# Kernel optimization log

Measured on AMD Instinct MI355X. Metric: run time of the kernel, lower is better.

## Reference

```python
import jax, jax.numpy as jnp
import numpy as np

B, N, HID = 2, 2048, 768
H, D, W = 12, 64, 128  # heads, head_dim, attention_half_width
P = 2 * W + 1          # number of relative-position buckets


def setup_inputs() -> dict:
    key = jax.random.key(0)
    ks = jax.random.split(key, 8)
    s = 0.02
    return {
        "hidden_states": jax.random.normal(ks[0], (B, N, HID), jnp.float32),
        "attention_mask": jnp.ones((B, N), jnp.bool_),
        "Wq": jax.random.normal(ks[1], (HID, HID), jnp.float32) * s,
        "Wk": jax.random.normal(ks[2], (HID, HID), jnp.float32) * s,
        "Wv": jax.random.normal(ks[3], (HID, HID), jnp.float32) * s,
        "position_query": jax.random.normal(ks[4], (1, H, D, P), jnp.float32),
        "position_key": jax.random.normal(ks[5], (1, H, D, P), jnp.float32),
        "Wo": jax.random.normal(ks[6], (HID, HID), jnp.float32) * s,
        "bo": jnp.zeros((HID,), jnp.float32),
    }


def reference(hidden_states, attention_mask, Wq, Wk, Wv, position_query, position_key, Wo, bo):
    b, n, hid = hidden_states.shape
    h, d, p = position_query.shape[1], position_query.shape[2], position_query.shape[3]
    w = (p - 1) // 2

    def split_heads(x):
        return x.reshape(b, n, h, d).transpose(0, 2, 1, 3)  # [B,H,N,D]

    q = split_heads(hidden_states @ Wq.T)
    k = split_heads(hidden_states @ Wk.T)
    v = split_heads(hidden_states @ Wv.T)

    # content-content scores (no sqrt(d) scaling in the original)
    score = jnp.einsum("bhid,bhjd->bhij", q, k)

    # relative position index: idx[i,j] = clip(j - i + w, 0, 2w)
    ids = jnp.arange(n)
    idx = jnp.clip(ids[None, :] - ids[:, None] + w, 0, 2 * w)  # [N,N] int32
    idx4 = idx[None, None]  # broadcast over B,H

    # content-to-position: gather over relative buckets
    c2p = jnp.einsum("bhid,hdp->bhip", q, position_key[0])  # [B,H,N,P]
    score = score + jnp.take_along_axis(c2p, idx4, axis=-1)

    # position-to-content: gather then transpose last two dims
    p2c = jnp.einsum("bhjd,hdp->bhjp", k, position_query[0])  # [B,H,N,P]
    score = score + jnp.swapaxes(jnp.take_along_axis(p2c, idx4, axis=-1), -1, -2)

    # band mask (|i-j| <= w) AND key/query validity masks
    band = jnp.abs(ids[:, None] - ids[None, :]) <= w  # [N,N]
    am = attention_mask.astype(jnp.bool_)
    mask = band[None, None] & am[:, None, None, :] & am[:, None, :, None]

    lv = jnp.finfo(score.dtype).min
    score = score + lv * (~mask).astype(score.dtype)  # additive masking, as in torch

    proba = jax.nn.softmax(score, axis=-1)
    context = jnp.einsum("bhij,bhjd->bhid", proba, v)
    context = context.transpose(0, 2, 1, 3).reshape(b, n, h * d)

    # VariationalNormalEpanechnikovDropout is identity in eval mode
    output = context @ Wo.T + bo
    return output, proba
```

## Files before the change

kernel.cpp:

```cpp
#include <hip/hip_runtime.h>
#include <math.h>

constexpr int kB   = 2;
constexpr int kN   = 2048;
constexpr int kHid = 768;
constexpr int kH   = 12;
constexpr int kD   = 64;
constexpr int kW   = 128;
constexpr int kP   = 2 * kW + 1;
constexpr int kPp  = 320;
constexpr int kM   = kB * kN;
constexpr int BHND = kB * kH * kN * kD;
constexpr int BHNP = kB * kH * kN * kP;

using f16 = _Float16;
typedef _Float16 f16x8 __attribute__((ext_vector_type(8)));
typedef _Float16 f16x4 __attribute__((ext_vector_type(4)));
typedef float    f32x4 __attribute__((ext_vector_type(4)));

__device__ __forceinline__ f16 f2h(float f) { return (f16)f; }
__device__ __forceinline__ float h2f(f16 h) { return (float)h; }
__device__ __forceinline__ void gload_lds16(const void* g, void* lds) {
  __builtin_amdgcn_global_load_lds((const __attribute__((address_space(1))) unsigned int*)g,
                                   (__attribute__((address_space(3))) unsigned int*)lds, 16, 0, 0);
}

__global__ __launch_bounds__(256) void castf2h(const float4* __restrict__ in,
                                               f16x4* __restrict__ out, int n4) {
  for (int i = blockIdx.x * 256 + threadIdx.x; i < n4; i += gridDim.x * 256) {
    const float4 f = in[i];
    f16x4 u;
    u[0] = f2h(f.x); u[1] = f2h(f.y); u[2] = f2h(f.z); u[3] = f2h(f.w);
    out[i] = u;
  }
}

__global__ __launch_bounds__(256) void cast4(const float* __restrict__ a, const float* __restrict__ b,
                                             const float* __restrict__ c, const float* __restrict__ d,
                                             f16* __restrict__ oa, f16* __restrict__ ob,
                                             f16* __restrict__ oc, f16* __restrict__ od) {
  const float* src[4] = {a, b, c, d};
  f16*         dst[4] = {oa, ob, oc, od};
  const int y = blockIdx.y;
  const int i = blockIdx.x * 256 + threadIdx.x;
  const float4 f = ((const float4*)src[y])[i];
  f16x4 u;
  u[0] = f2h(f.x); u[1] = f2h(f.y); u[2] = f2h(f.z); u[3] = f2h(f.w);
  ((f16x4*)dst[y])[i] = u;
}

__global__ __launch_bounds__(256) void postrans(const float* __restrict__ pq, const float* __restrict__ pk,
                                                f16* __restrict__ pqt, f16* __restrict__ pkt) {
  const float* s = blockIdx.y ? pk : pq;
  f16*         o = blockIdx.y ? pkt : pqt;
  const int idx = blockIdx.x * 256 + threadIdx.x;
  const int h = idx / (kPp * kD);
  const int rem = idx % (kPp * kD);
  const int p = rem >> 6, d = rem & 63;
  const float v = (p < kP) ? s[((size_t)h * kD + d) * kP + p] : 0.f;
  o[idx] = f2h(v);
}

template <int MODE>
__global__ __launch_bounds__(256) void gemm_mfma(const f16* __restrict__ A,
                                                 const f16* __restrict__ Bt,
                                                 const float* __restrict__ bias,
                                                 float* __restrict__ outF,
                                                 f16* __restrict__ outB) {
  __shared__ f16 Ab[2][64 * 32];
  __shared__ f16 Bb[2][64 * 32];
  const int tid = threadIdx.x;
  const int lane = tid & 63, wave = tid >> 6;
  const int wm = wave >> 1, wn = wave & 1;
  const int m0 = blockIdx.y * 64, c0 = blockIdx.x * 64;

  const int srow = tid >> 2, sseg = (tid & 3) * 8;
  const f16* gA = A + (size_t)(m0 + srow) * kHid + sseg;
  const f16* gB = Bt + (size_t)(c0 + srow) * kHid + sseg;

  f32x4 acc[2][2] = {};
  const int fr = lane & 15, fk = (lane >> 4) * 8;

  gload_lds16(gA, &Ab[0][wave * 512]);
  gload_lds16(gB, &Bb[0][wave * 512]);
  __syncthreads();

  int cur = 0;
  for (int t = 0; t < 24; ++t) {
    if (t < 23) {
      gload_lds16(gA + (t + 1) * 32, &Ab[cur ^ 1][wave * 512]);
      gload_lds16(gB + (t + 1) * 32, &Bb[cur ^ 1][wave * 512]);
    }
    const f16x8 a0 = *(const f16x8*)&Ab[cur][(wm * 32 + fr) * 32 + fk];
    const f16x8 a1 = *(const f16x8*)&Ab[cur][(wm * 32 + 16 + fr) * 32 + fk];
    const f16x8 b0 = *(const f16x8*)&Bb[cur][(wn * 32 + fr) * 32 + fk];
    const f16x8 b1 = *(const f16x8*)&Bb[cur][(wn * 32 + 16 + fr) * 32 + fk];
    acc[0][0] = __builtin_amdgcn_mfma_f32_16x16x32_f16(a0, b0, acc[0][0], 0, 0, 0);
    acc[0][1] = __builtin_amdgcn_mfma_f32_16x16x32_f16(a0, b1, acc[0][1], 0, 0, 0);
    acc[1][0] = __builtin_amdgcn_mfma_f32_16x16x32_f16(a1, b0, acc[1][0], 0, 0, 0);
    acc[1][1] = __builtin_amdgcn_mfma_f32_16x16x32_f16(a1, b1, acc[1][1], 0, 0, 0);
    __syncthreads();
    cur ^= 1;
  }

  const int orow0 = m0 + wm * 32 + (lane >> 4) * 4;
  const int ocol0 = c0 + wn * 32 + (lane & 15);
#pragma unroll
  for (int m16 = 0; m16 < 2; ++m16)
#pragma unroll
    for (int n16 = 0; n16 < 2; ++n16)
#pragma unroll
      for (int rg = 0; rg < 4; ++rg) {
        const int m = orow0 + m16 * 16 + rg;
        const int cc = ocol0 + n16 * 16;
        const float val = acc[m16][n16][rg];
        if (MODE == 1) {
          outF[(size_t)m * kHid + cc] = val + bias[cc];
        } else {
          const int b = m >> 11, n = m & 2047;
          const int hh = cc >> 6, d = cc & 63;
          const size_t o = (((size_t)b * kH + hh) * kN + n) * kD + d;
          outF[o] = val;
          if (MODE == 2) outB[o] = f2h(val);
        }
      }
}

__global__ __launch_bounds__(256) void posgemm_mfma(const f16* __restrict__ src,
                                                    const f16* __restrict__ posT,
                                                    f16* __restrict__ outp) {
  __shared__ f16 Ab[64 * 64];
  __shared__ f16 Bb[64 * 64];
  const int tid = threadIdx.x;
  const int lane = tid & 63, wave = tid >> 6;
  const int wm = wave >> 1, wn = wave & 1;
  const int p0 = blockIdx.x * 64, n0 = blockIdx.y * 64, bh = blockIdx.z;
  const int h = bh % kH;

  const f16* gA = src + ((size_t)bh * kN + n0) * kD;
  const f16* gB = posT + ((size_t)h * kPp + p0) * kD;
#pragma unroll
  for (int ps = 0; ps < 2; ++ps) {
    const int idx = ps * 256 + tid;
    gload_lds16(gA + idx * 8, &Ab[ps * 2048 + wave * 512]);
    gload_lds16(gB + idx * 8, &Bb[ps * 2048 + wave * 512]);
  }
  __syncthreads();

  f32x4 acc[2][2] = {};
  const int fr = lane & 15, fk = (lane >> 4) * 8;
#pragma unroll
  for (int ks = 0; ks < 2; ++ks) {
    const int k0 = ks * 32;
    const f16x8 a0 = *(const f16x8*)&Ab[(wm * 32 + fr) * 64 + k0 + fk];
    const f16x8 a1 = *(const f16x8*)&Ab[(wm * 32 + 16 + fr) * 64 + k0 + fk];
    const f16x8 b0 = *(const f16x8*)&Bb[(wn * 32 + fr) * 64 + k0 + fk];
    const f16x8 b1 = *(const f16x8*)&Bb[(wn * 32 + 16 + fr) * 64 + k0 + fk];
    acc[0][0] = __builtin_amdgcn_mfma_f32_16x16x32_f16(a0, b0, acc[0][0], 0, 0, 0);
    acc[0][1] = __builtin_amdgcn_mfma_f32_16x16x32_f16(a0, b1, acc[0][1], 0, 0, 0);
    acc[1][0] = __builtin_amdgcn_mfma_f32_16x16x32_f16(a1, b0, acc[1][0], 0, 0, 0);
    acc[1][1] = __builtin_amdgcn_mfma_f32_16x16x32_f16(a1, b1, acc[1][1], 0, 0, 0);
  }

  const int nrow0 = n0 + wm * 32 + (lane >> 4) * 4;
  const int pcol0 = p0 + wn * 32 + (lane & 15);
#pragma unroll
  for (int m16 = 0; m16 < 2; ++m16)
#pragma unroll
    for (int n16 = 0; n16 < 2; ++n16)
#pragma unroll
      for (int rg = 0; rg < 4; ++rg) {
        const int n = nrow0 + m16 * 16 + rg;
        const int p = pcol0 + n16 * 16;
        if (p < kP) outp[((size_t)bh * kN + n) * kP + p] = f2h(acc[m16][n16][rg]);
      }
}

constexpr int KS  = 72;
constexpr int SBs = 296;

__global__ __launch_bounds__(256) void attn_tile(const float* __restrict__ q,
                                                 const float* __restrict__ k,
                                                 const float* __restrict__ v,
                                                 const f16* __restrict__ c2p,
                                                 const f16* __restrict__ p2c,
                                                 float* __restrict__ proba,
                                                 float* __restrict__ ctx) {
  __shared__ f16 kbuf[288 * KS];
  __shared__ float sbuf[32 * SBs];
  __shared__ float inv_s[32];
  const int tid = threadIdx.x;
  const int i0 = blockIdx.x * 32;
  const int h = blockIdx.y, b = blockIdx.z;
  const size_t bh = (size_t)b * kH + h;

  const int jlo = (i0 - kW > 0) ? (i0 - kW) : 0;
  const int jhi = (i0 + 31 + kW < kN - 1) ? (i0 + 31 + kW) : (kN - 1);
  const int bw = jhi - jlo + 1;

  {
    const float* kg = k + (bh * kN + jlo) * kD;
    for (int idx = tid; idx < bw * 16; idx += 256) {
      const int row = idx >> 4, seg = (idx & 15) << 2;
      const float4 f = *(const float4*)(kg + (size_t)row * kD + seg);
      f16x4 u;
      u[0] = f2h(f.x); u[1] = f2h(f.y); u[2] = f2h(f.z); u[3] = f2h(f.w);
      *(f16x4*)&kbuf[row * KS + seg] = u;
    }
  }
  __syncthreads();

  const int g = tid >> 4, tx = tid & 15;
  const f16* p2cb = p2c + bh * kN * (size_t)kP;

#pragma unroll
  for (int rr = 0; rr < 2; ++rr) {
    const int r = g + 16 * rr;
    const int i_r = i0 + r;

    float qv[64];
    const float* qp = q + (bh * kN + i_r) * kD;
#pragma unroll
    for (int m = 0; m < 16; ++m) {
      const float4 f = *(const float4*)(qp + 4 * m);
      qv[4 * m] = f.x; qv[4 * m + 1] = f.y; qv[4 * m + 2] = f.z; qv[4 * m + 3] = f.w;
    }
    const f16* c2pr = c2p + (bh * kN + i_r) * kP;

    for (int c = tx; c < bw; c += 16) {
      const int j = jlo + c;
      const int dij = j - i_r;
      float s;
      if (dij >= -kW && dij <= kW) {
        const f16* kp = &kbuf[c * KS];
        float s0 = 0.f, s1 = 0.f, s2 = 0.f, s3 = 0.f;
#pragma unroll
        for (int m = 0; m < 8; ++m) {
          const f16x8 kv = *(const f16x8*)(kp + 8 * m);
          s0 = fmaf(qv[8 * m + 0], h2f(kv[0]), s0);
          s1 = fmaf(qv[8 * m + 1], h2f(kv[1]), s1);
          s2 = fmaf(qv[8 * m + 2], h2f(kv[2]), s2);
          s3 = fmaf(qv[8 * m + 3], h2f(kv[3]), s3);
          s0 = fmaf(qv[8 * m + 4], h2f(kv[4]), s0);
          s1 = fmaf(qv[8 * m + 5], h2f(kv[5]), s1);
          s2 = fmaf(qv[8 * m + 6], h2f(kv[6]), s2);
          s3 = fmaf(qv[8 * m + 7], h2f(kv[7]), s3);
        }
        s = (s0 + s1) + (s2 + s3);
        s += h2f(c2pr[dij + kW]) + h2f(p2cb[(size_t)j * kP + (kW - dij)]);
      } else {
        s = -INFINITY;
      }
      sbuf[r * SBs + c] = s;
    }

    float mx = -INFINITY;
    for (int c = tx; c < bw; c += 16) mx = fmaxf(mx, sbuf[r * SBs + c]);
#pragma unroll
    for (int d = 8; d >= 1; d >>= 1) mx = fmaxf(mx, __shfl_xor(mx, d, 16));
    float sum = 0.f;
    for (int c = tx; c < bw; c += 16) {
      const float e = __expf(sbuf[r * SBs + c] - mx);
      sbuf[r * SBs + c] = e;
      sum += e;
    }
#pragma unroll
    for (int d = 8; d >= 1; d >>= 1) sum += __shfl_xor(sum, d, 16);
    const float inv = 1.f / sum;
    if (tx == 0) inv_s[r] = inv;

    {
      float a0 = 0.f, a1 = 0.f, a2 = 0.f, a3 = 0.f;
      const float* vb = v + (bh * kN + jlo) * kD + (tx << 2);
#pragma unroll 4
      for (int c = 0; c < bw; ++c) {
        const float p = sbuf[r * SBs + c];
        const float4 v4 = *(const float4*)(vb + (size_t)c * kD);
        a0 = fmaf(p, v4.x, a0);
        a1 = fmaf(p, v4.y, a1);
        a2 = fmaf(p, v4.z, a2);
        a3 = fmaf(p, v4.w, a3);
      }
      float4 o; o.x = a0 * inv; o.y = a1 * inv; o.z = a2 * inv; o.w = a3 * inv;
      *(float4*)(ctx + ((size_t)b * kN + i_r) * kHid + h * kD + (tx << 2)) = o;
    }
  }
  __syncthreads();

  float* pbase = proba + (bh * kN + i0) * (size_t)kN;
  for (int rr = 0; rr < 32; ++rr) {
    const int irr = i0 + rr;
    const float innv = inv_s[rr];
    const int lo2 = (irr - kW > 0) ? (irr - kW) : 0;
    const int hi2 = (irr + kW < kN - 1) ? (irr + kW) : (kN - 1);
    float* prow = pbase + (size_t)rr * kN;
    for (int c4 = tid; c4 < kN / 4; c4 += 256) {
      const int j0 = c4 << 2;
      float4 o;
      float* ov = (float*)&o;
#pragma unroll
      for (int e = 0; e < 4; ++e) {
        const int j = j0 + e;
        ov[e] = (j >= lo2 && j <= hi2) ? sbuf[rr * SBs + (j - jlo)] * innv : 0.f;
      }
      *(float4*)(prow + j0) = o;
    }
  }
}

extern "C" void kernel_launch(void* const* d_in, const int* in_sizes, int n_in,
                              void* d_out, int out_size, void* d_ws, size_t ws_size,
                              hipStream_t stream) {
  const float* X  = (const float*)d_in[0];
  const float* Wq = (const float*)d_in[2];
  const float* Wk = (const float*)d_in[3];
  const float* Wv = (const float*)d_in[4];
  const float* PQ = (const float*)d_in[5];
  const float* PK = (const float*)d_in[6];
  const float* Wo = (const float*)d_in[7];
  const float* bo = (const float*)d_in[8];

  float* out   = (float*)d_out;
  float* proba = out + (size_t)kB * kN * kHid;

  float* qws = (float*)d_ws;
  float* kws = qws + BHND;
  float* vws = kws + BHND;
  float* ctx = vws + BHND;
  f16* c2p = (f16*)(ctx + (size_t)kB * kN * kHid);
  f16* p2c = c2p + (size_t)BHNP;
  f16* Xb  = p2c + (size_t)BHNP;
  f16* Wqb = Xb + (size_t)kM * kHid;
  f16* Wkb = Wqb + kHid * kHid;
  f16* Wvb = Wkb + kHid * kHid;
  f16* Wob = Wvb + kHid * kHid;
  f16* qb  = Wob + kHid * kHid;
  f16* kb  = qb + (size_t)BHND;
  f16* PQt = kb + (size_t)BHND;
  f16* PKt = PQt + kH * kPp * kD;
  f16* ctxb = Xb;

  castf2h<<<1024, 256, 0, stream>>>((const float4*)X, (f16x4*)Xb, kM * kHid / 4);
  cast4<<<dim3(576, 4), 256, 0, stream>>>(Wq, Wk, Wv, Wo, Wqb, Wkb, Wvb, Wob);
  postrans<<<dim3(960, 2), 256, 0, stream>>>(PQ, PK, PQt, PKt);

  const dim3 ggrid(kHid / 64, kM / 64);
  gemm_mfma<2><<<ggrid, 256, 0, stream>>>(Xb, Wqb, nullptr, qws, qb);
  gemm_mfma<2><<<ggrid, 256, 0, stream>>>(Xb, Wkb, nullptr, kws, kb);
  gemm_mfma<0><<<ggrid, 256, 0, stream>>>(Xb, Wvb, nullptr, vws, nullptr);

  const dim3 pgrid(kPp / 64, kN / 64, kB * kH);
  posgemm_mfma<<<pgrid, 256, 0, stream>>>(qb, PKt, c2p);
  posgemm_mfma<<<pgrid, 256, 0, stream>>>(kb, PQt, p2c);

  attn_tile<<<dim3(kN / 32, kH, kB), 256, 0, stream>>>(qws, kws, vws, c2p, p2c, proba, ctx);

  castf2h<<<1024, 256, 0, stream>>>((const float4*)ctx, (f16x4*)ctxb, kM * kHid / 4);
  gemm_mfma<1><<<ggrid, 256, 0, stream>>>(ctxb, Wob, bo, out, nullptr);
}
```

Baseline: 761.2 us.

## Fuse prep casts, QKV GEMMs and pos-GEMMs; use f16 Q/K with fdot2 in attention

Merges the three cast/transpose kernels into one prep kernel, fuses the Q/K/V projections into one 128x128-tile GEMM with swizzled LDS, and merges the two positional GEMMs into one launch. The attention kernel now reads f16 Q/K through async global-to-LDS loads with an XOR swizzle, computes dot products with fdot2, remaps block order, writes ctx directly in f16 (dropping the separate cast), and uses nontemporal stores for proba. These changes cut launch count, fp32 intermediate traffic and conversion work. In exchange, Q in the QK dot product is now rounded to f16, which adds some precision loss.

```diff
diff --git a/kernel.cpp b/kernel.cpp
--- a/kernel.cpp
+++ b/kernel.cpp
@@ -16,7 +16,14 @@
 using f16 = _Float16;
 typedef _Float16 f16x8 __attribute__((ext_vector_type(8)));
 typedef _Float16 f16x4 __attribute__((ext_vector_type(4)));
+typedef _Float16 f16x2 __attribute__((ext_vector_type(2)));
 typedef float    f32x4 __attribute__((ext_vector_type(4)));
+
+#if defined(__has_builtin)
+#if __has_builtin(__builtin_amdgcn_fdot2)
+#define HAVE_FDOT2 1
+#endif
+#endif
 
 __device__ __forceinline__ f16 f2h(float f) { return (f16)f; }
 __device__ __forceinline__ float h2f(f16 h) { return (float)h; }
@@ -25,117 +32,148 @@
                                    (__attribute__((address_space(3))) unsigned int*)lds, 16, 0, 0);
 }
 
-__global__ __launch_bounds__(256) void castf2h(const float4* __restrict__ in,
-                                               f16x4* __restrict__ out, int n4) {
-  for (int i = blockIdx.x * 256 + threadIdx.x; i < n4; i += gridDim.x * 256) {
-    const float4 f = in[i];
-    f16x4 u;
-    u[0] = f2h(f.x); u[1] = f2h(f.y); u[2] = f2h(f.z); u[3] = f2h(f.w);
-    out[i] = u;
-  }
-}
-
-__global__ __launch_bounds__(256) void cast4(const float* __restrict__ a, const float* __restrict__ b,
-                                             const float* __restrict__ c, const float* __restrict__ d,
-                                             f16* __restrict__ oa, f16* __restrict__ ob,
-                                             f16* __restrict__ oc, f16* __restrict__ od) {
-  const float* src[4] = {a, b, c, d};
-  f16*         dst[4] = {oa, ob, oc, od};
-  const int y = blockIdx.y;
-  const int i = blockIdx.x * 256 + threadIdx.x;
-  const float4 f = ((const float4*)src[y])[i];
-  f16x4 u;
-  u[0] = f2h(f.x); u[1] = f2h(f.y); u[2] = f2h(f.z); u[3] = f2h(f.w);
-  ((f16x4*)dst[y])[i] = u;
-}
-
-__global__ __launch_bounds__(256) void postrans(const float* __restrict__ pq, const float* __restrict__ pk,
-                                                f16* __restrict__ pqt, f16* __restrict__ pkt) {
-  const float* s = blockIdx.y ? pk : pq;
-  f16*         o = blockIdx.y ? pkt : pqt;
-  const int idx = blockIdx.x * 256 + threadIdx.x;
-  const int h = idx / (kPp * kD);
-  const int rem = idx % (kPp * kD);
-  const int p = rem >> 6, d = rem & 63;
-  const float v = (p < kP) ? s[((size_t)h * kD + d) * kP + p] : 0.f;
-  o[idx] = f2h(v);
+__global__ __launch_bounds__(256) void prep(const float* __restrict__ X,
+                                            const float* __restrict__ Wq, const float* __restrict__ Wk,
+                                            const float* __restrict__ Wv, const float* __restrict__ Wo,
+                                            const float* __restrict__ PQ, const float* __restrict__ PK,
+                                            f16* __restrict__ Xb, f16* __restrict__ Wqkvb,
+                                            f16* __restrict__ Wob, f16* __restrict__ PQt,
+                                            f16* __restrict__ PKt) {
+  const int bid = blockIdx.x, tid = threadIdx.x;
+  if (bid < 3072) {
+    const int i = bid * 256 + tid;
+    const float4 f = ((const float4*)X)[i];
+    f16x4 u; u[0] = f2h(f.x); u[1] = f2h(f.y); u[2] = f2h(f.z); u[3] = f2h(f.w);
+    ((f16x4*)Xb)[i] = u;
+  } else if (bid < 5376) {
+    const int i = (bid - 3072) * 256 + tid;
+    const int which = i / 147456, r = i % 147456;
+    const float* Ws[4] = {Wq, Wk, Wv, Wo};
+    const float4 f = ((const float4*)Ws[which])[r];
+    f16x4 u; u[0] = f2h(f.x); u[1] = f2h(f.y); u[2] = f2h(f.z); u[3] = f2h(f.w);
+    if (which < 3) ((f16x4*)Wqkvb)[which * 147456 + r] = u;
+    else           ((f16x4*)Wob)[r] = u;
+  } else {
+    const int i = (bid - 5376) * 256 + tid;
+    const int y = i / 245760, rem = i % 245760;
+    const int h = rem / (kPp * kD), rem2 = rem % (kPp * kD);
+    const int p = rem2 >> 6, d = rem2 & 63;
+    const float* s = y ? PK : PQ;
+    f16* o = y ? PKt : PQt;
+    const float vv = (p < kP) ? s[((size_t)h * kD + d) * kP + p] : 0.f;
+    o[rem] = f2h(vv);
+  }
 }
 
 template <int MODE>
-__global__ __launch_bounds__(256) void gemm_mfma(const f16* __restrict__ A,
-                                                 const f16* __restrict__ Bt,
-                                                 const float* __restrict__ bias,
-                                                 float* __restrict__ outF,
-                                                 f16* __restrict__ outB) {
-  __shared__ f16 Ab[2][64 * 32];
-  __shared__ f16 Bb[2][64 * 32];
-  const int tid = threadIdx.x;
-  const int lane = tid & 63, wave = tid >> 6;
+__global__ __launch_bounds__(256) void gemm128(const f16* __restrict__ A,
+                                               const f16* __restrict__ Bt,
+                                               const float* __restrict__ bias,
+                                               f16* __restrict__ qb, f16* __restrict__ kb,
+                                               float* __restrict__ vws,
+                                               float* __restrict__ outF) {
+  constexpr int K = kHid;
+  __shared__ f16 Ab[2][128 * 32];
+  __shared__ f16 Bb[2][128 * 32];
+  const int tid = threadIdx.x, lane = tid & 63, wave = tid >> 6;
   const int wm = wave >> 1, wn = wave & 1;
-  const int m0 = blockIdx.y * 64, c0 = blockIdx.x * 64;
-
-  const int srow = tid >> 2, sseg = (tid & 3) * 8;
-  const f16* gA = A + (size_t)(m0 + srow) * kHid + sseg;
-  const f16* gB = Bt + (size_t)(c0 + srow) * kHid + sseg;
-
-  f32x4 acc[2][2] = {};
-  const int fr = lane & 15, fk = (lane >> 4) * 8;
-
-  gload_lds16(gA, &Ab[0][wave * 512]);
-  gload_lds16(gB, &Bb[0][wave * 512]);
+  const int m0 = blockIdx.y * 128, c0 = blockIdx.x * 128;
+
+  const f16* gA[2]; const f16* gB[2];
+#pragma unroll
+  for (int c = 0; c < 2; ++c) {
+    const int row = (wave * 2 + c) * 16 + (lane >> 2);
+    const int seg = (lane & 3) ^ ((row >> 1) & 3);
+    gA[c] = A + (size_t)(m0 + row) * K + seg * 8;
+    gB[c] = Bt + (size_t)(c0 + row) * K + seg * 8;
+  }
+
+  const int fr = lane & 15, fks = lane >> 4;
+  int aoff[4], boff[4];
+#pragma unroll
+  for (int i = 0; i < 4; ++i) {
+    const int ra = wm * 64 + i * 16 + fr;
+    aoff[i] = ra * 32 + ((fks ^ ((ra >> 1) & 3)) << 3);
+    const int rb = wn * 64 + i * 16 + fr;
+    boff[i] = rb * 32 + ((fks ^ ((rb >> 1) & 3)) << 3);
+  }
+
+  f32x4 acc[4][4] = {};
+
+#pragma unroll
+  for (int c = 0; c < 2; ++c) {
+    gload_lds16(gA[c], &Ab[0][wave * 1024 + c * 512]);
+    gload_lds16(gB[c], &Bb[0][wave * 1024 + c * 512]);
+  }
   __syncthreads();
 
   int cur = 0;
   for (int t = 0; t < 24; ++t) {
     if (t < 23) {
-      gload_lds16(gA + (t + 1) * 32, &Ab[cur ^ 1][wave * 512]);
-      gload_lds16(gB + (t + 1) * 32, &Bb[cur ^ 1][wave * 512]);
-    }
-    const f16x8 a0 = *(const f16x8*)&Ab[cur][(wm * 32 + fr) * 32 + fk];
-    const f16x8 a1 = *(const f16x8*)&Ab[cur][(wm * 32 + 16 + fr) * 32 + fk];
-    const f16x8 b0 = *(const f16x8*)&Bb[cur][(wn * 32 + fr) * 32 + fk];
-    const f16x8 b1 = *(const f16x8*)&Bb[cur][(wn * 32 + 16 + fr) * 32 + fk];
-    acc[0][0] = __builtin_amdgcn_mfma_f32_16x16x32_f16(a0, b0, acc[0][0], 0, 0, 0);
-    acc[0][1] = __builtin_amdgcn_mfma_f32_16x16x32_f16(a0, b1, acc[0][1], 0, 0, 0);
-    acc[1][0] = __builtin_amdgcn_mfma_f32_16x16x32_f16(a1, b0, acc[1][0], 0, 0, 0);
-    acc[1][1] = __builtin_amdgcn_mfma_f32_16x16x32_f16(a1, b1, acc[1][1], 0, 0, 0);
+#pragma unroll
+      for (int c = 0; c < 2; ++c) {
+        gload_lds16(gA[c] + (t + 1) * 32, &Ab[cur ^ 1][wave * 1024 + c * 512]);
+        gload_lds16(gB[c] + (t + 1) * 32, &Bb[cur ^ 1][wave * 1024 + c * 512]);
+      }
+    }
+    f16x8 af[4], bf[4];
+#pragma unroll
+    for (int i = 0; i < 4; ++i) af[i] = *(const f16x8*)&Ab[cur][aoff[i]];
+#pragma unroll
+    for (int i = 0; i < 4; ++i) bf[i] = *(const f16x8*)&Bb[cur][boff[i]];
+#pragma unroll
+    for (int mi = 0; mi < 4; ++mi)
+#pragma unroll
+      for (int ni = 0; ni < 4; ++ni)
+        acc[mi][ni] = __builtin_amdgcn_mfma_f32_16x16x32_f16(af[mi], bf[ni], acc[mi][ni], 0, 0, 0);
     __syncthreads();
     cur ^= 1;
   }
 
-  const int orow0 = m0 + wm * 32 + (lane >> 4) * 4;
-  const int ocol0 = c0 + wn * 32 + (lane & 15);
-#pragma unroll
-  for (int m16 = 0; m16 < 2; ++m16)
-#pragma unroll
-    for (int n16 = 0; n16 < 2; ++n16)
+  const int orow0 = m0 + wm * 64 + (lane >> 4) * 4;
+  const int ocol0 = c0 + wn * 64 + fr;
+  const int sel = (MODE == 0) ? (c0 >= 1536 ? 2 : (c0 >= 768 ? 1 : 0)) : 0;
+#pragma unroll
+  for (int mi = 0; mi < 4; ++mi)
+#pragma unroll
+    for (int ni = 0; ni < 4; ++ni)
 #pragma unroll
       for (int rg = 0; rg < 4; ++rg) {
-        const int m = orow0 + m16 * 16 + rg;
-        const int cc = ocol0 + n16 * 16;
-        const float val = acc[m16][n16][rg];
+        const int m = orow0 + mi * 16 + rg;
+        const int cc = ocol0 + ni * 16;
+        const float val = acc[mi][ni][rg];
         if (MODE == 1) {
           outF[(size_t)m * kHid + cc] = val + bias[cc];
         } else {
+          const int cd = cc - sel * 768;
           const int b = m >> 11, n = m & 2047;
-          const int hh = cc >> 6, d = cc & 63;
+          const int hh = cd >> 6, d = cd & 63;
           const size_t o = (((size_t)b * kH + hh) * kN + n) * kD + d;
-          outF[o] = val;
-          if (MODE == 2) outB[o] = f2h(val);
+          if (sel == 0)      qb[o] = f2h(val);
+          else if (sel == 1) kb[o] = f2h(val);
+          else               vws[o] = val;
         }
       }
 }
 
-__global__ __launch_bounds__(256) void posgemm_mfma(const f16* __restrict__ src,
-                                                    const f16* __restrict__ posT,
-                                                    f16* __restrict__ outp) {
+__global__ __launch_bounds__(256) void posgemm_mfma(const f16* __restrict__ qb,
+                                                    const f16* __restrict__ kb,
+                                                    const f16* __restrict__ PKt,
+                                                    const f16* __restrict__ PQt,
+                                                    f16* __restrict__ c2p,
+                                                    f16* __restrict__ p2c) {
   __shared__ f16 Ab[64 * 64];
   __shared__ f16 Bb[64 * 64];
   const int tid = threadIdx.x;
   const int lane = tid & 63, wave = tid >> 6;
   const int wm = wave >> 1, wn = wave & 1;
-  const int p0 = blockIdx.x * 64, n0 = blockIdx.y * 64, bh = blockIdx.z;
+  const int p0 = blockIdx.x * 64, n0 = blockIdx.y * 64;
+  const int z = blockIdx.z;
+  const int bh = (z < 24) ? z : z - 24;
   const int h = bh % kH;
+  const f16* src  = (z < 24) ? qb : kb;
+  const f16* posT = (z < 24) ? PKt : PQt;
+  f16* outp       = (z < 24) ? c2p : p2c;
 
   const f16* gA = src + ((size_t)bh * kN + n0) * kD;
   const f16* gB = posT + ((size_t)h * kPp + p0) * kD;
@@ -176,22 +214,24 @@
       }
 }
 
-constexpr int KS  = 72;
 constexpr int SBs = 296;
 
-__global__ __launch_bounds__(256) void attn_tile(const float* __restrict__ q,
-                                                 const float* __restrict__ k,
+__global__ __launch_bounds__(256) void attn_tile(const f16* __restrict__ qg,
+                                                 const f16* __restrict__ kg,
                                                  const float* __restrict__ v,
                                                  const f16* __restrict__ c2p,
                                                  const f16* __restrict__ p2c,
                                                  float* __restrict__ proba,
-                                                 float* __restrict__ ctx) {
-  __shared__ f16 kbuf[288 * KS];
+                                                 f16* __restrict__ ctxb) {
+  __shared__ f16 kbuf[288 * 64];
   __shared__ float sbuf[32 * SBs];
   __shared__ float inv_s[32];
   const int tid = threadIdx.x;
-  const int i0 = blockIdx.x * 32;
-  const int h = blockIdx.y, b = blockIdx.z;
+  int lin = blockIdx.x;
+  lin = (lin & 7) * 192 + (lin >> 3);
+  const int i0 = (lin & 63) * 32;
+  const int h  = (lin >> 6) % kH;
+  const int b  = lin / 768;
   const size_t bh = (size_t)b * kH + h;
 
   const int jlo = (i0 - kW > 0) ? (i0 - kW) : 0;
@@ -199,13 +239,15 @@
   const int bw = jhi - jlo + 1;
 
   {
-    const float* kg = k + (bh * kN + jlo) * kD;
-    for (int idx = tid; idx < bw * 16; idx += 256) {
-      const int row = idx >> 4, seg = (idx & 15) << 2;
-      const float4 f = *(const float4*)(kg + (size_t)row * kD + seg);
-      f16x4 u;
-      u[0] = f2h(f.x); u[1] = f2h(f.y); u[2] = f2h(f.z); u[3] = f2h(f.w);
-      *(f16x4*)&kbuf[row * KS + seg] = u;
+    const int wave = tid >> 6, lane = tid & 63;
+#pragma unroll
+    for (int c = 0; c < 9; ++c) {
+      const int qq = wave * 9 + c;
+      const int slot = qq * 64 + lane;
+      const int row = slot >> 3, t = slot & 7;
+      int j = jlo + row; if (j > kN - 1) j = kN - 1;
+      const f16* src = kg + ((size_t)bh * kN + j) * kD + ((t ^ (row & 7)) << 3);
+      gload_lds16(src, &kbuf[qq * 512]);
     }
   }
   __syncthreads();
@@ -218,36 +260,42 @@
     const int r = g + 16 * rr;
     const int i_r = i0 + r;
 
-    float qv[64];
-    const float* qp = q + (bh * kN + i_r) * kD;
-#pragma unroll
-    for (int m = 0; m < 16; ++m) {
-      const float4 f = *(const float4*)(qp + 4 * m);
-      qv[4 * m] = f.x; qv[4 * m + 1] = f.y; qv[4 * m + 2] = f.z; qv[4 * m + 3] = f.w;
+    f16x2 qh[32];
+    {
+      const f16x8* qp8 = (const f16x8*)(qg + (bh * kN + i_r) * (size_t)kD);
+#pragma unroll
+      for (int m = 0; m < 8; ++m) {
+        union { f16x8 v8; f16x2 h2[4]; } u; u.v8 = qp8[m];
+#pragma unroll
+        for (int e = 0; e < 4; ++e) qh[m * 4 + e] = u.h2[e];
+      }
     }
     const f16* c2pr = c2p + (bh * kN + i_r) * kP;
 
     for (int c = tx; c < bw; c += 16) {
-      const int j = jlo + c;
-      const int dij = j - i_r;
+      const int dij = jlo + c - i_r;
       float s;
       if (dij >= -kW && dij <= kW) {
-        const f16* kp = &kbuf[c * KS];
-        float s0 = 0.f, s1 = 0.f, s2 = 0.f, s3 = 0.f;
+        const f16* kp = &kbuf[c * 64];
+        float s0 = 0.f, s1 = 0.f;
 #pragma unroll
         for (int m = 0; m < 8; ++m) {
-          const f16x8 kv = *(const f16x8*)(kp + 8 * m);
-          s0 = fmaf(qv[8 * m + 0], h2f(kv[0]), s0);
-          s1 = fmaf(qv[8 * m + 1], h2f(kv[1]), s1);
-          s2 = fmaf(qv[8 * m + 2], h2f(kv[2]), s2);
-          s3 = fmaf(qv[8 * m + 3], h2f(kv[3]), s3);
-          s0 = fmaf(qv[8 * m + 4], h2f(kv[4]), s0);
-          s1 = fmaf(qv[8 * m + 5], h2f(kv[5]), s1);
-          s2 = fmaf(qv[8 * m + 6], h2f(kv[6]), s2);
-          s3 = fmaf(qv[8 * m + 7], h2f(kv[7]), s3);
+          union { f16x8 v8; f16x2 h2[4]; } u;
+          u.v8 = *(const f16x8*)(kp + ((m ^ (c & 7)) << 3));
+#ifdef HAVE_FDOT2
+          s0 = __builtin_amdgcn_fdot2(u.h2[0], qh[m * 4 + 0], s0, false);
+          s1 = __builtin_amdgcn_fdot2(u.h2[1], qh[m * 4 + 1], s1, false);
+          s0 = __builtin_amdgcn_fdot2(u.h2[2], qh[m * 4 + 2], s0, false);
+          s1 = __builtin_amdgcn_fdot2(u.h2[3], qh[m * 4 + 3], s1, false);
+#else
+#pragma unroll
+          for (int e = 0; e < 4; ++e) {
+            s0 = fmaf(h2f(u.h2[e][0]), h2f(qh[m * 4 + e][0]), s0);
+            s1 = fmaf(h2f(u.h2[e][1]), h2f(qh[m * 4 + e][1]), s1);
+          }
+#endif
         }
-        s = (s0 + s1) + (s2 + s3);
-        s += h2f(c2pr[dij + kW]) + h2f(p2cb[(size_t)j * kP + (kW - dij)]);
+        s = s0 + s1 + h2f(c2pr[dij + kW]) + h2f(p2cb[(size_t)(jlo + c) * kP + (kW - dij)]);
       } else {
         s = -INFINITY;
       }
@@ -281,8 +329,9 @@
         a2 = fmaf(p, v4.z, a2);
         a3 = fmaf(p, v4.w, a3);
       }
-      float4 o; o.x = a0 * inv; o.y = a1 * inv; o.z = a2 * inv; o.w = a3 * inv;
-      *(float4*)(ctx + ((size_t)b * kN + i_r) * kHid + h * kD + (tx << 2)) = o;
+      f16x4 o;
+      o[0] = f2h(a0 * inv); o[1] = f2h(a1 * inv); o[2] = f2h(a2 * inv); o[3] = f2h(a3 * inv);
+      *(f16x4*)(ctxb + ((size_t)b * kN + i_r) * kHid + h * kD + (tx << 2)) = o;
     }
   }
   __syncthreads();
@@ -296,14 +345,13 @@
     float* prow = pbase + (size_t)rr * kN;
     for (int c4 = tid; c4 < kN / 4; c4 += 256) {
       const int j0 = c4 << 2;
-      float4 o;
-      float* ov = (float*)&o;
+      f32x4 o;
 #pragma unroll
       for (int e = 0; e < 4; ++e) {
         const int j = j0 + e;
-        ov[e] = (j >= lo2 && j <= hi2) ? sbuf[rr * SBs + (j - jlo)] * innv : 0.f;
-      }
-      *(float4*)(prow + j0) = o;
+        o[e] = (j >= lo2 && j <= hi2) ? sbuf[rr * SBs + (j - jlo)] * innv : 0.f;
+      }
+      __builtin_nontemporal_store(o, (f32x4*)(prow + j0));
     }
   }
 }
@@ -323,38 +371,25 @@
   float* out   = (float*)d_out;
   float* proba = out + (size_t)kB * kN * kHid;
 
-  float* qws = (float*)d_ws;
-  float* kws = qws + BHND;
-  float* vws = kws + BHND;
-  float* ctx = vws + BHND;
-  f16* c2p = (f16*)(ctx + (size_t)kB * kN * kHid);
-  f16* p2c = c2p + (size_t)BHNP;
-  f16* Xb  = p2c + (size_t)BHNP;
-  f16* Wqb = Xb + (size_t)kM * kHid;
-  f16* Wkb = Wqb + kHid * kHid;
-  f16* Wvb = Wkb + kHid * kHid;
-  f16* Wob = Wvb + kHid * kHid;
-  f16* qb  = Wob + kHid * kHid;
-  f16* kb  = qb + (size_t)BHND;
-  f16* PQt = kb + (size_t)BHND;
-  f16* PKt = PQt + kH * kPp * kD;
-  f16* ctxb = Xb;
-
-  castf2h<<<1024, 256, 0, stream>>>((const float4*)X, (f16x4*)Xb, kM * kHid / 4);
-  cast4<<<dim3(576, 4), 256, 0, stream>>>(Wq, Wk, Wv, Wo, Wqb, Wkb, Wvb, Wob);
-  postrans<<<dim3(960, 2), 256, 0, stream>>>(PQ, PK, PQt, PKt);
-
-  const dim3 ggrid(kHid / 64, kM / 64);
-  gemm_mfma<2><<<ggrid, 256, 0, stream>>>(Xb, Wqb, nullptr, qws, qb);
-  gemm_mfma<2><<<ggrid, 256, 0, stream>>>(Xb, Wkb, nullptr, kws, kb);
-  gemm_mfma<0><<<ggrid, 256, 0, stream>>>(Xb, Wvb, nullptr, vws, nullptr);
-
-  const dim3 pgrid(kPp / 64, kN / 64, kB * kH);
-  posgemm_mfma<<<pgrid, 256, 0, stream>>>(qb, PKt, c2p);
-  posgemm_mfma<<<pgrid, 256, 0, stream>>>(kb, PQt, p2c);
-
-  attn_tile<<<dim3(kN / 32, kH, kB), 256, 0, stream>>>(qws, kws, vws, c2p, p2c, proba, ctx);
-
-  castf2h<<<1024, 256, 0, stream>>>((const float4*)ctx, (f16x4*)ctxb, kM * kHid / 4);
-  gemm_mfma<1><<<ggrid, 256, 0, stream>>>(ctxb, Wob, bo, out, nullptr);
-}
+  float* vws = (float*)d_ws;
+  f16* qb    = (f16*)(vws + BHND);
+  f16* kb    = qb + (size_t)BHND;
+  f16* c2p   = kb + (size_t)BHND;
+  f16* p2c   = c2p + (size_t)BHNP;
+  f16* Xb    = p2c + (size_t)BHNP;
+  f16* Wqkvb = Xb + (size_t)kM * kHid;
+  f16* Wob   = Wqkvb + (size_t)3 * kHid * kHid;
+  f16* PQt   = Wob + (size_t)kHid * kHid;
+  f16* PKt   = PQt + kH * kPp * kD;
+  f16* ctxb  = PKt + kH * kPp * kD;
+
+  prep<<<7296, 256, 0, stream>>>(X, Wq, Wk, Wv, Wo, PQ, PK, Xb, Wqkvb, Wob, PQt, PKt);
+
+  gemm128<0><<<dim3(18, 32), 256, 0, stream>>>(Xb, Wqkvb, nullptr, qb, kb, vws, nullptr);
+
+  posgemm_mfma<<<dim3(kPp / 64, kN / 64, 48), 256, 0, stream>>>(qb, kb, PKt, PQt, c2p, p2c);
+
+  attn_tile<<<1536, 256, 0, stream>>>(qb, kb, vws, c2p, p2c, proba, ctxb);
+
+  gemm128<1><<<dim3(6, 32), 256, 0, stream>>>(ctxb, Wob, bo, nullptr, nullptr, nullptr, out);
+}
```

Measured after the change: 649.8 us. 1.17x faster.
